# Kernel tuning notes

Hardware: AMD Instinct MI355X
Metric: run time of the kernel (lower is better)

The kernel has to match this reference:

```python
import math
import jax, jax.numpy as jnp
import numpy as np


def setup_inputs() -> dict:
    key = jax.random.key(0)
    bs, n_tok, n_heads, width = 2, 2048, 4, 64
    WIN = 64  # window size == dst_mxlen; every dst row exactly full
    k1, k2, k3 = jax.random.split(key, 3)
    q = jax.random.normal(k1, (bs, n_tok, n_heads, width), jnp.float32)
    k_ = jax.random.normal(k2, (bs, n_tok, n_heads, width), jnp.float32)
    v = jax.random.normal(k3, (bs, n_tok, n_heads, width), jnp.float32)
    d = np.arange(n_tok)
    j = np.arange(WIN)
    dst = np.repeat(d, WIN)                                   # [cl]
    src = ((d[:, None] + j[None, :] - WIN // 2) % n_tok).reshape(-1)
    cnt = np.tile(j, n_tok)
    coo = jnp.asarray(np.stack([dst, src, cnt], axis=1), jnp.int32)  # [cl, 3]
    return {"v": v, "q": q, "k": k_, "coo": coo, "dst_mxlen": WIN, "src_mxlen": WIN}


def reference(v, q, k, coo, dst_mxlen, src_mxlen):
    bs, n_tok, n_heads, width = q.shape
    dst, src, cnt = coo[:, 0], coo[:, 1], coo[:, 2]
    scale = -1.0 / math.sqrt(width)
    # permute to [b, h, n_tok, w], gather along token axis
    qq = q.transpose(0, 2, 1, 3)[:, :, dst, :]   # [b, h, cl, w]
    kk = k.transpose(0, 2, 1, 3)[:, :, src, :]   # [b, h, cl, w]
    ww = jnp.sum(jnp.abs(qq - kk), axis=-1) * scale  # L1 scores [b, h, cl]
    NEG = jnp.asarray(-1e12, q.dtype)
    attn = jnp.full((bs, n_heads, n_tok, dst_mxlen), NEG, q.dtype)
    attn = attn.at[:, :, dst, cnt].set(ww)       # scatter into padded buffer
    attn_sm = jax.nn.softmax(attn, axis=-1)      # [b, h, n_tok, dst_mxlen]
    # gather normalized weights back at coo positions; padded slots would
    # multiply zeros in the original vw buffer, so segment-accumulating only
    # filled entries is exactly the same math as the dense einsum.
    w = attn_sm[:, :, dst, cnt]                  # [b, h, cl]
    vv = v.transpose(0, 2, 1, 3)[:, :, src, :]   # [b, h, cl, w]
    vo = jnp.zeros((bs, n_heads, n_tok, width), q.dtype)
    vo = vo.at[:, :, dst, :].add(w[..., None] * vv)
    return vo.transpose(0, 2, 1, 3)              # [b, n_tok, h, w]
```

## Files before the change

### kernel.cpp

```cpp
#include <hip/hip_runtime.h>

#define BS    2
#define NTOK  2048
#define NH    4
#define W     64
#define HALF  32
#define DTILE 16
#define ND    4
#define NROW  17
#define ROWS  80
#define RSTRIDE 64

template<int CTRL>
__device__ __forceinline__ float fadd_dpp(float x) {
    int y = __builtin_amdgcn_mov_dpp(__float_as_int(x), CTRL, 0xF, 0xF, true);
    return x + __int_as_float(y);
}

__global__ __launch_bounds__(256, 4) void l1attn_win64_v5(
    const float* __restrict__ v,
    const float* __restrict__ q,
    const float* __restrict__ k,
    float* __restrict__ out)
{
    __shared__ alignas(16) float ks[ROWS * RSTRIDE];
    __shared__ alignas(16) float vs[ROWS * RSTRIDE];

    const int tid  = threadIdx.x;
    const int lane = tid & 63;
    const int widx = tid >> 6;

    int bid = blockIdx.x;
    bid = (bid & 7) * 128 + (bid >> 3);

    const int bh = bid >> 7;
    const int d0 = (bid & 127) * DTILE;
    const int h  = bh & (NH - 1);
    const int b  = bh >> 2;
    const int base = b * (NTOK * NH * W) + h * W;

    #pragma unroll
    for (int i = 0; i < 5; ++i) {
        const int row   = (i * 4096 + tid * 16) >> 8;
        const int chunk = tid & 15;
        const int src   = (d0 - HALF + row) & (NTOK - 1);
        const float* gk = k + base + src * (NH * W) + chunk * 4;
        const float* gv = v + base + src * (NH * W) + chunk * 4;
        char* lk = (char*)ks + i * 4096 + widx * 1024;
        char* lv = (char*)vs + i * 4096 + widx * 1024;
        __builtin_amdgcn_global_load_lds(
            (const __attribute__((address_space(1))) void*)gk,
            (__attribute__((address_space(3))) void*)lk, 16, 0, 0);
        __builtin_amdgcn_global_load_lds(
            (const __attribute__((address_space(1))) void*)gv,
            (__attribute__((address_space(3))) void*)lv, 16, 0, 0);
    }

    const int l16 = lane & 15;
    const int r   = lane >> 4;
    const int c0  = l16 * 4;
    const int dw0 = d0 + widx * ND;

    float4 qv[ND];
    #pragma unroll
    for (int dd = 0; dd < ND; ++dd)
        qv[dd] = *(const float4*)(q + base + (dw0 + dd) * (NH * W) + c0);

    __syncthreads();

    float4 acc[ND];
    float  ssum[ND];
    #pragma unroll
    for (int dd = 0; dd < ND; ++dd) {
        acc[dd] = make_float4(0.f, 0.f, 0.f, 0.f);
        ssum[dd] = 0.f;
    }

    const float SC = -0.125f * 1.44269504088896f;
    const int lr0 = widx * ND + r;

    #pragma unroll
    for (int it = 0; it < NROW; ++it) {
        const int lrow = lr0 + it * 4;
        const float4 kv = *(const float4*)&ks[lrow * RSTRIDE + c0];
        const float4 vv = *(const float4*)&vs[lrow * RSTRIDE + c0];
        #pragma unroll
        for (int dd = 0; dd < ND; ++dd) {
            float t = fabsf(qv[dd].x - kv.x) + fabsf(qv[dd].y - kv.y)
                    + fabsf(qv[dd].z - kv.z) + fabsf(qv[dd].w - kv.w);
            t = fadd_dpp<0xB1>(t);
            t = fadd_dpp<0x4E>(t);
            t = fadd_dpp<0x141>(t);
            t = fadd_dpp<0x128>(t);
            float sc = t * SC;
            if (it == 0)        sc = (r <  dd) ? -1e30f : sc;
            if (it == NROW - 1) sc = (r >= dd) ? -1e30f : sc;
            const float p = __builtin_amdgcn_exp2f(sc);
            ssum[dd] += p;
            acc[dd].x = fmaf(p, vv.x, acc[dd].x);
            acc[dd].y = fmaf(p, vv.y, acc[dd].y);
            acc[dd].z = fmaf(p, vv.z, acc[dd].z);
            acc[dd].w = fmaf(p, vv.w, acc[dd].w);
        }
    }

    #pragma unroll
    for (int dd = 0; dd < ND; ++dd) {
        ssum[dd] += __shfl_xor(ssum[dd], 16);
        ssum[dd] += __shfl_xor(ssum[dd], 32);
        acc[dd].x += __shfl_xor(acc[dd].x, 16);
        acc[dd].y += __shfl_xor(acc[dd].y, 16);
        acc[dd].z += __shfl_xor(acc[dd].z, 16);
        acc[dd].w += __shfl_xor(acc[dd].w, 16);
        acc[dd].x += __shfl_xor(acc[dd].x, 32);
        acc[dd].y += __shfl_xor(acc[dd].y, 32);
        acc[dd].z += __shfl_xor(acc[dd].z, 32);
        acc[dd].w += __shfl_xor(acc[dd].w, 32);
    }
    if (r == 0) {
        #pragma unroll
        for (int dd = 0; dd < ND; ++dd) {
            const float inv = 1.0f / ssum[dd];
            *(float4*)(out + base + (dw0 + dd) * (NH * W) + c0) =
                make_float4(acc[dd].x * inv, acc[dd].y * inv,
                            acc[dd].z * inv, acc[dd].w * inv);
        }
    }
}

extern "C" void kernel_launch(void* const* d_in, const int* in_sizes, int n_in,
                              void* d_out, int out_size, void* d_ws, size_t ws_size,
                              hipStream_t stream) {
    const float* v = (const float*)d_in[0];
    const float* q = (const float*)d_in[1];
    const float* k = (const float*)d_in[2];
    float* out = (float*)d_out;

    const int blocks = (BS * NH * NTOK) / DTILE;
    hipLaunchKernelGGL(l1attn_win64_v5, dim3(blocks), dim3(256), 0, stream,
                       v, q, k, out);
}
```

Baseline: 16.02 us.

## Split each 16-destination tile across eight waves of two rows each

Doubles the block to 512 threads (8 waves) and halves the destination rows per wave from 4 to 2, keeping the same 16-row tile per block. The K and V staging is merged into a single shared buffer, filled by one async global-to-LDS load per iteration instead of two. A row clamp keeps the padded last iteration inside the 80-row buffer. The aim is more waves in flight and fewer live registers to hide latency better. The cost is twice as many LDS reads of K/V rows per destination and more cross-lane reduction work per useful output.

```diff
diff --git a/kernel.cpp b/kernel.cpp
--- a/kernel.cpp
+++ b/kernel.cpp
@@ -6,10 +6,10 @@
 #define W     64
 #define HALF  32
 #define DTILE 16
-#define ND    4
+#define ND    2
 #define NROW  17
 #define ROWS  80
-#define RSTRIDE 64
+#define NWAVE 8
 
 template<int CTRL>
 __device__ __forceinline__ float fadd_dpp(float x) {
@@ -17,14 +17,13 @@
     return x + __int_as_float(y);
 }
 
-__global__ __launch_bounds__(256, 4) void l1attn_win64_v5(
+__global__ __launch_bounds__(512, 8) void l1attn_win64_v6(
     const float* __restrict__ v,
     const float* __restrict__ q,
     const float* __restrict__ k,
     float* __restrict__ out)
 {
-    __shared__ alignas(16) float ks[ROWS * RSTRIDE];
-    __shared__ alignas(16) float vs[ROWS * RSTRIDE];
+    __shared__ alignas(16) float smem[2 * ROWS * W];
 
     const int tid  = threadIdx.x;
     const int lane = tid & 63;
@@ -41,19 +40,17 @@
 
     #pragma unroll
     for (int i = 0; i < 5; ++i) {
-        const int row   = (i * 4096 + tid * 16) >> 8;
-        const int chunk = tid & 15;
-        const int src   = (d0 - HALF + row) & (NTOK - 1);
-        const float* gk = k + base + src * (NH * W) + chunk * 4;
-        const float* gv = v + base + src * (NH * W) + chunk * 4;
-        char* lk = (char*)ks + i * 4096 + widx * 1024;
-        char* lv = (char*)vs + i * 4096 + widx * 1024;
+        const int c    = i * 512 + tid;
+        const int row  = c >> 4;
+        const int sub  = c & 15;
+        const int isV  = (row >= ROWS);
+        const int trow = isV ? row - ROWS : row;
+        const int src  = (d0 - HALF + trow) & (NTOK - 1);
+        const float* g = (isV ? v : k) + base + src * (NH * W) + sub * 4;
+        char* l = (char*)smem + (i * 512 + widx * 64) * 16;
         __builtin_amdgcn_global_load_lds(
-            (const __attribute__((address_space(1))) void*)gk,
-            (__attribute__((address_space(3))) void*)lk, 16, 0, 0);
-        __builtin_amdgcn_global_load_lds(
-            (const __attribute__((address_space(1))) void*)gv,
-            (__attribute__((address_space(3))) void*)lv, 16, 0, 0);
+            (const __attribute__((address_space(1))) void*)g,
+            (__attribute__((address_space(3))) void*)l, 16, 0, 0);
     }
 
     const int l16 = lane & 15;
@@ -81,9 +78,10 @@
 
     #pragma unroll
     for (int it = 0; it < NROW; ++it) {
-        const int lrow = lr0 + it * 4;
-        const float4 kv = *(const float4*)&ks[lrow * RSTRIDE + c0];
-        const float4 vv = *(const float4*)&vs[lrow * RSTRIDE + c0];
+        int lrow = lr0 + it * 4;
+        lrow = lrow > (ROWS - 1) ? (ROWS - 1) : lrow;
+        const float4 kv = *(const float4*)&smem[lrow * W + c0];
+        const float4 vv = *(const float4*)&smem[(ROWS + lrow) * W + c0];
         #pragma unroll
         for (int dd = 0; dd < ND; ++dd) {
             float t = fabsf(qv[dd].x - kv.x) + fabsf(qv[dd].y - kv.y)
@@ -137,6 +135,6 @@
     float* out = (float*)d_out;
 
     const int blocks = (BS * NH * NTOK) / DTILE;
-    hipLaunchKernelGGL(l1attn_win64_v5, dim3(blocks), dim3(256), 0, stream,
+    hipLaunchKernelGGL(l1attn_win64_v6, dim3(blocks), dim3(512), 0, stream,
                        v, q, k, out);
 }
```

New measurement: 33.14 us. +106.9%, slower.
